# Kernel tuning notes

Measured on AMD Instinct MI355X. Metric: run time of the kernel, lower is better.

## Reference

```python
import jax, jax.numpy as jnp
import numpy as np

T, B, D = 4096, 64, 64
SCALE = D ** (-0.5)


def setup_inputs() -> dict:
    key = jax.random.key(0)
    ks = jax.random.split(key, 8)
    init = 1.0 / np.sqrt(D)  # mimic nn.Linear default scale roughly
    return {
        "eeg": jax.random.normal(ks[0], (T, B, D), dtype=jnp.float32),
        "fnirs": jax.random.normal(ks[1], (T, B, D), dtype=jnp.float32),
        "Wq": jax.random.normal(ks[2], (D, D), dtype=jnp.float32) * init,
        "bq": jax.random.normal(ks[3], (D,), dtype=jnp.float32) * init,
        "Wk": jax.random.normal(ks[4], (D, D), dtype=jnp.float32) * init,
        "bk": jax.random.normal(ks[5], (D,), dtype=jnp.float32) * init,
        "Wv": jax.random.normal(ks[6], (D, D), dtype=jnp.float32) * init,
        "bv": jax.random.normal(ks[7], (D,), dtype=jnp.float32) * init,
    }


def reference(eeg, fnirs, Wq, bq, Wk, bk, Wv, bv):
    # Linear layers: x @ W.T + b (torch nn.Linear convention, W is [out, in])
    q = jnp.einsum("tbd,od->tbo", eeg, Wq) + bq      # [T, B, D]
    k = jnp.einsum("tbd,od->tbo", fnirs, Wk) + bk    # [T, B, D]
    v = jnp.einsum("tbd,od->tbo", fnirs, Wv) + bv    # [T, B, D]
    # Elementwise QK gating score, summed over feature dim -> [T, B, 1]
    score = jnp.sum(q * k, axis=-1, keepdims=True) * SCALE
    # Softmax over the sequence axis (dim=0)
    attn = jax.nn.softmax(score, axis=0)
    # Residual combine
    return eeg + attn * v
```

## Files before the change

kernel.cpp:

```cpp
#include <hip/hip_runtime.h>
#include <hip/hip_bf16.h>
#include <math.h>

#define T_DIM 4096
#define B_DIM 64
#define NROWS (T_DIM * B_DIM)
#define NTILES (NROWS / 16)

#define WS_MFRAG 0
#define WS_VFRAG 2048
#define WS_U     4096
#define WS_W     4160
#define WS_C     4224
#define WS_MX    4240
#define WS_INV   4304
#define WS_PM    4368
#define WS_PS    8464
#define WS_SCORE 16384

typedef __attribute__((ext_vector_type(4))) float f32x4;
typedef __attribute__((ext_vector_type(8))) short bf16x8;

static __device__ inline short f2bf(float x) {
  __hip_bfloat16 h = __float2bfloat16(x);
  return *reinterpret_cast<short*>(&h);
}

static __device__ inline bf16x8 cvt8(const float4 a, const float4 b) {
  bf16x8 r;
  r[0] = f2bf(a.x); r[1] = f2bf(a.y); r[2] = f2bf(a.z); r[3] = f2bf(a.w);
  r[4] = f2bf(b.x); r[5] = f2bf(b.y); r[6] = f2bf(b.z); r[7] = f2bf(b.w);
  return r;
}

static __device__ inline float dot4(const float4 a, const float4 b, float acc) {
  acc = fmaf(a.x, b.x, acc); acc = fmaf(a.y, b.y, acc);
  acc = fmaf(a.z, b.z, acc); acc = fmaf(a.w, b.w, acc);
  return acc;
}

static __device__ __host__ inline int frag_idx(int d, int k) {
  return ((d >> 4) * 2 + (k >> 5)) * 512 +
         ((((k >> 3) & 3) * 16 + (d & 15)) * 8) + (k & 7);
}

__global__ __launch_bounds__(64) void k1_precompute(
    const float* __restrict__ Wq, const float* __restrict__ bq,
    const float* __restrict__ Wk, const float* __restrict__ bk,
    const float* __restrict__ Wv, float* __restrict__ ws) {
  const int tid = threadIdx.x;
  const int blk = blockIdx.x;
  unsigned short* __restrict__ mfrag = (unsigned short*)(ws + WS_MFRAG);
  unsigned short* __restrict__ vfrag = (unsigned short*)(ws + WS_VFRAG);
  if (blk < 64) {
    const int d = blk;
    float acc = 0.f;
#pragma unroll
    for (int o = 0; o < 64; ++o)
      acc = fmaf(Wq[o * 64 + d], Wk[o * 64 + tid], acc);
    const int idx = frag_idx(d, tid);
    mfrag[idx] = (unsigned short)f2bf(acc);
    vfrag[idx] = (unsigned short)f2bf(Wv[d * 64 + tid]);
  } else {
    float uacc = 0.f, wacc = 0.f, cacc = 0.f;
#pragma unroll
    for (int o = 0; o < 64; ++o) {
      uacc = fmaf(bq[o], Wk[o * 64 + tid], uacc);
      wacc = fmaf(Wq[o * 64 + tid], bk[o], wacc);
      cacc = fmaf(bq[o], bk[o], cacc);
    }
    ws[WS_U + tid] = uacc;
    ws[WS_W + tid] = wacc;
    if (tid == 0) ws[WS_C] = cacc;
  }
}

__global__ __launch_bounds__(256, 2) void k2_score_mfma(
    const float* __restrict__ eeg, const float* __restrict__ fnirs,
    const unsigned short* __restrict__ mfrag, const float* __restrict__ wvec,
    const float* __restrict__ uvec, const float* __restrict__ cvec,
    float* __restrict__ score) {
  __shared__ float lds[4][1024];
  const int tid = threadIdx.x;
  const int lane = tid & 63;
  const int wv = tid >> 6;
  const int tile = blockIdx.x * 4 + wv;
  const int c = lane & 15;
  const int g = lane >> 4;
  const int rbase = tile * 16;
  float* L = lds[wv];

  const float* Fb = fnirs + (size_t)rbase * 64;
  const float* Eb = eeg + (size_t)rbase * 64;
  float4 Fj[4], Ej[4];
#pragma unroll
  for (int j = 0; j < 4; ++j)
    Fj[j] = *reinterpret_cast<const float4*>(Fb + j * 256 + lane * 4);
#pragma unroll
  for (int j = 0; j < 4; ++j)
    Ej[j] = *reinterpret_cast<const float4*>(Eb + j * 256 + lane * 4);
  bf16x8 bm[4][2];
#pragma unroll
  for (int dt = 0; dt < 4; ++dt)
#pragma unroll
    for (int kf = 0; kf < 2; ++kf)
      bm[dt][kf] = *reinterpret_cast<const bf16x8*>(
          mfrag + (((dt * 2 + kf) << 9) + lane * 8));
  float4 wf[4];
#pragma unroll
  for (int dt = 0; dt < 4; ++dt)
    wf[dt] = *reinterpret_cast<const float4*>(wvec + dt * 16 + g * 4);
  const float4 u4 = *reinterpret_cast<const float4*>(uvec + c * 4);
  const float cb = cvec[0];
  __builtin_amdgcn_sched_barrier(0);

  float uf[4];
#pragma unroll
  for (int j = 0; j < 4; ++j) uf[j] = dot4(Fj[j], u4, 0.f);

#pragma unroll
  for (int j = 0; j < 4; ++j) {
    const int r = j * 4 + g;
    const int addr = r * 64 + ((((c >> 1) ^ (r & 7)) << 3) + ((c & 1) << 2));
    *reinterpret_cast<float4*>(&L[addr]) = Fj[j];
  }
  const int fr0 = c * 64 + (((g) ^ (c & 7)) << 3);
  const int fr1 = c * 64 + (((4 + g) ^ (c & 7)) << 3);
  const float4 p00 = *reinterpret_cast<const float4*>(&L[fr0]);
  const float4 p01 = *reinterpret_cast<const float4*>(&L[fr0 + 4]);
  const float4 p10 = *reinterpret_cast<const float4*>(&L[fr1]);
  const float4 p11 = *reinterpret_cast<const float4*>(&L[fr1 + 4]);
  const bf16x8 a0 = cvt8(p00, p01);
  const bf16x8 a1 = cvt8(p10, p11);

  const f32x4 zero = {0.f, 0.f, 0.f, 0.f};
  f32x4 acc[4];
#pragma unroll
  for (int dt = 0; dt < 4; ++dt) {
    acc[dt] = __builtin_amdgcn_mfma_f32_16x16x32_bf16(bm[dt][0], a0, zero, 0, 0, 0);
    acc[dt] = __builtin_amdgcn_mfma_f32_16x16x32_bf16(bm[dt][1], a1, acc[dt], 0, 0, 0);
  }

#pragma unroll
  for (int dt = 0; dt < 4; ++dt) {
    float4 hp;
    hp.x = acc[dt][0] + wf[dt].x; hp.y = acc[dt][1] + wf[dt].y;
    hp.z = acc[dt][2] + wf[dt].z; hp.w = acc[dt][3] + wf[dt].w;
    const int ch = dt * 2 + (g >> 1);
    const int addr = c * 64 + (((ch ^ (c & 7)) << 3) + ((g & 1) << 2));
    *reinterpret_cast<float4*>(&L[addr]) = hp;
  }
#pragma unroll
  for (int j = 0; j < 4; ++j) {
    const int r = j * 4 + g;
    const int addr = r * 64 + ((((c >> 1) ^ (r & 7)) << 3) + ((c & 1) << 2));
    const float4 hp = *reinterpret_cast<const float4*>(&L[addr]);
    float p = dot4(Ej[j], hp, uf[j]);
    p += __shfl_xor(p, 1, 64);
    p += __shfl_xor(p, 2, 64);
    p += __shfl_xor(p, 4, 64);
    p += __shfl_xor(p, 8, 64);
    if (c == 0) score[rbase + j * 4 + g] = (p + cb) * 0.125f;
  }
}

__global__ __launch_bounds__(256) void k3a_partial(
    const float* __restrict__ sc, float* __restrict__ pm,
    float* __restrict__ ps) {
  __shared__ float sm[4][64], ss[4][64];
  const int tid = threadIdx.x;
  const int b = tid & 63;
  const int tq = tid >> 6;
  const int t0 = blockIdx.x * 64;
  float m = -1e30f, s = 0.f;
#pragma unroll
  for (int k = 0; k < 16; ++k) {
    const float v = sc[(size_t)(t0 + k * 4 + tq) * 64 + b];
    const float mn = fmaxf(m, v);
    s = s * __expf(m - mn) + __expf(v - mn);
    m = mn;
  }
  sm[tq][b] = m; ss[tq][b] = s;
  __syncthreads();
  if (tid < 64) {
    float M = sm[0][b], S = ss[0][b];
#pragma unroll
    for (int w = 1; w < 4; ++w) {
      const float m2 = sm[w][b], s2 = ss[w][b];
      const float Mn = fmaxf(M, m2);
      S = S * __expf(M - Mn) + s2 * __expf(m2 - Mn);
      M = Mn;
    }
    pm[blockIdx.x * 64 + b] = M;
    ps[blockIdx.x * 64 + b] = S;
  }
}

__global__ __launch_bounds__(64) void k3b_combine(
    const float* __restrict__ pm, const float* __restrict__ ps,
    float* __restrict__ mx, float* __restrict__ inv) {
  const int b = threadIdx.x;
  float M = pm[b], S = ps[b];
#pragma unroll
  for (int ck = 1; ck < 64; ++ck) {
    const float m2 = pm[ck * 64 + b], s2 = ps[ck * 64 + b];
    const float Mn = fmaxf(M, m2);
    S = S * __expf(M - Mn) + s2 * __expf(m2 - Mn);
    M = Mn;
  }
  mx[b] = M;
  inv[b] = 1.0f / S;
}

__global__ __launch_bounds__(256, 2) void k4_output_mfma(
    const float* __restrict__ eeg, const float* __restrict__ fnirs,
    const unsigned short* __restrict__ vfrag, const float* __restrict__ bv,
    const float* __restrict__ score, const float* __restrict__ mx,
    const float* __restrict__ inv, float* __restrict__ out) {
  __shared__ float lds[4][1024];
  const int tid = threadIdx.x;
  const int lane = tid & 63;
  const int wv = tid >> 6;
  const int tile = blockIdx.x * 4 + wv;
  const int c = lane & 15;
  const int g = lane >> 4;
  const int rbase = tile * 16;
  float* L = lds[wv];

  const float* Fb = fnirs + (size_t)rbase * 64;
  const float* Eb = eeg + (size_t)rbase * 64;
  float4 Fj[4], Ej[4];
#pragma unroll
  for (int j = 0; j < 4; ++j)
    Fj[j] = *reinterpret_cast<const float4*>(Fb + j * 256 + lane * 4);
#pragma unroll
  for (int j = 0; j < 4; ++j)
    Ej[j] = *reinterpret_cast<const float4*>(Eb + j * 256 + lane * 4);
  bf16x8 bm[4][2];
#pragma unroll
  for (int dt = 0; dt < 4; ++dt)
#pragma unroll
    for (int kf = 0; kf < 2; ++kf)
      bm[dt][kf] = *reinterpret_cast<const bf16x8*>(
          vfrag + (((dt * 2 + kf) << 9) + lane * 8));
  float4 bvf[4];
#pragma unroll
  for (int dt = 0; dt < 4; ++dt)
    bvf[dt] = *reinterpret_cast<const float4*>(bv + dt * 16 + g * 4);
  const float scr = score[rbase + c];
  const int bidx = (rbase + c) & 63;
  const float mxv = mx[bidx];
  const float invv = inv[bidx];
  __builtin_amdgcn_sched_barrier(0);

#pragma unroll
  for (int j = 0; j < 4; ++j) {
    const int r = j * 4 + g;
    const int addr = r * 64 + ((((c >> 1) ^ (r & 7)) << 3) + ((c & 1) << 2));
    *reinterpret_cast<float4*>(&L[addr]) = Fj[j];
  }
  const int fr0 = c * 64 + (((g) ^ (c & 7)) << 3);
  const int fr1 = c * 64 + (((4 + g) ^ (c & 7)) << 3);
  const float4 p00 = *reinterpret_cast<const float4*>(&L[fr0]);
  const float4 p01 = *reinterpret_cast<const float4*>(&L[fr0 + 4]);
  const float4 p10 = *reinterpret_cast<const float4*>(&L[fr1]);
  const float4 p11 = *reinterpret_cast<const float4*>(&L[fr1 + 4]);
  const bf16x8 a0 = cvt8(p00, p01);
  const bf16x8 a1 = cvt8(p10, p11);

  const f32x4 zero = {0.f, 0.f, 0.f, 0.f};
  f32x4 acc[4];
#pragma unroll
  for (int dt = 0; dt < 4; ++dt) {
    acc[dt] = __builtin_amdgcn_mfma_f32_16x16x32_bf16(bm[dt][0], a0, zero, 0, 0, 0);
    acc[dt] = __builtin_amdgcn_mfma_f32_16x16x32_bf16(bm[dt][1], a1, acc[dt], 0, 0, 0);
  }

  const float aC = __expf(scr - mxv) * invv;
#pragma unroll
  for (int dt = 0; dt < 4; ++dt) {
    float4 v4;
    v4.x = aC * (acc[dt][0] + bvf[dt].x); v4.y = aC * (acc[dt][1] + bvf[dt].y);
    v4.z = aC * (acc[dt][2] + bvf[dt].z); v4.w = aC * (acc[dt][3] + bvf[dt].w);
    const int ch = dt * 2 + (g >> 1);
    const int addr = c * 64 + (((ch ^ (c & 7)) << 3) + ((g & 1) << 2));
    *reinterpret_cast<float4*>(&L[addr]) = v4;
  }
  float* Ob = out + (size_t)rbase * 64;
#pragma unroll
  for (int j = 0; j < 4; ++j) {
    const int r = j * 4 + g;
    const int addr = r * 64 + ((((c >> 1) ^ (r & 7)) << 3) + ((c & 1) << 2));
    const float4 v = *reinterpret_cast<const float4*>(&L[addr]);
    float4 o;
    o.x = Ej[j].x + v.x; o.y = Ej[j].y + v.y;
    o.z = Ej[j].z + v.z; o.w = Ej[j].w + v.w;
    *reinterpret_cast<float4*>(Ob + j * 256 + lane * 4) = o;
  }
}

extern "C" void kernel_launch(void* const* d_in, const int* in_sizes, int n_in,
                              void* d_out, int out_size, void* d_ws, size_t ws_size,
                              hipStream_t stream) {
  const float* eeg   = (const float*)d_in[0];
  const float* fnirs = (const float*)d_in[1];
  const float* Wq    = (const float*)d_in[2];
  const float* bq    = (const float*)d_in[3];
  const float* Wk    = (const float*)d_in[4];
  const float* bk    = (const float*)d_in[5];
  const float* Wv    = (const float*)d_in[6];
  const float* bv    = (const float*)d_in[7];
  float* out = (float*)d_out;
  float* ws  = (float*)d_ws;

  k1_precompute<<<65, 64, 0, stream>>>(Wq, bq, Wk, bk, Wv, ws);
  k2_score_mfma<<<NTILES / 4, 256, 0, stream>>>(
      eeg, fnirs, (const unsigned short*)(ws + WS_MFRAG), ws + WS_W,
      ws + WS_U, ws + WS_C, ws + WS_SCORE);
  k3a_partial<<<64, 256, 0, stream>>>(ws + WS_SCORE, ws + WS_PM, ws + WS_PS);
  k3b_combine<<<1, 64, 0, stream>>>(ws + WS_PM, ws + WS_PS,
                                    ws + WS_MX, ws + WS_INV);
  k4_output_mfma<<<NTILES / 4, 256, 0, stream>>>(
      eeg, fnirs, (const unsigned short*)(ws + WS_VFRAG), bv,
      ws + WS_SCORE, ws + WS_MX, ws + WS_INV, out);
}
```

Before: 66.65 us.

## Process four tiles per wave with double-buffered register prefetch in score and output kernels

Each wave in the score and output kernels now handles four consecutive 16-row tiles instead of one. The next tile's eeg/fnirs loads are issued before the current tile is computed, using two register buffers. This amortizes the per-wave setup (weight fragment and bias loads) and overlaps global memory latency with MFMA work. In exchange the grid is four times smaller and register pressure rises, which may reduce occupancy and the memory parallelism available across the GPU.

After: 69.50 us. 1.04x slower.

```diff
diff --git a/kernel.cpp b/kernel.cpp
--- a/kernel.cpp
+++ b/kernel.cpp
@@ -75,6 +75,62 @@
   }
 }
 
+
+#define K2_LOAD(Fj, Ej, t)                                                   \
+  {                                                                          \
+    const float* Fb_ = fnirs + (size_t)(t) * 1024;                           \
+    const float* Eb_ = eeg + (size_t)(t) * 1024;                             \
+    _Pragma("unroll") for (int j = 0; j < 4; ++j)                            \
+        Fj[j] = *reinterpret_cast<const float4*>(Fb_ + j * 256 + lane * 4);  \
+    _Pragma("unroll") for (int j = 0; j < 4; ++j)                            \
+        Ej[j] = *reinterpret_cast<const float4*>(Eb_ + j * 256 + lane * 4);  \
+  }
+
+#define K2_COMP(Fj, Ej, t)                                                   \
+  {                                                                          \
+    const int rbase_ = (t) * 16;                                             \
+    float uf_[4];                                                            \
+    _Pragma("unroll") for (int j = 0; j < 4; ++j)                            \
+        uf_[j] = dot4(Fj[j], u4, 0.f);                                       \
+    _Pragma("unroll") for (int j = 0; j < 4; ++j) {                          \
+      const int r_ = j * 4 + g;                                              \
+      const int a_ = r_ * 64 + ((((c >> 1) ^ (r_ & 7)) << 3) + ((c & 1) << 2)); \
+      *reinterpret_cast<float4*>(&L[a_]) = Fj[j];                            \
+    }                                                                        \
+    const int fr0_ = c * 64 + (((g) ^ (c & 7)) << 3);                        \
+    const int fr1_ = c * 64 + (((4 + g) ^ (c & 7)) << 3);                    \
+    const float4 p00_ = *reinterpret_cast<const float4*>(&L[fr0_]);          \
+    const float4 p01_ = *reinterpret_cast<const float4*>(&L[fr0_ + 4]);      \
+    const float4 p10_ = *reinterpret_cast<const float4*>(&L[fr1_]);          \
+    const float4 p11_ = *reinterpret_cast<const float4*>(&L[fr1_ + 4]);      \
+    const bf16x8 a0_ = cvt8(p00_, p01_);                                     \
+    const bf16x8 a1_ = cvt8(p10_, p11_);                                     \
+    f32x4 acc_[4];                                                           \
+    _Pragma("unroll") for (int dt = 0; dt < 4; ++dt) {                       \
+      acc_[dt] = __builtin_amdgcn_mfma_f32_16x16x32_bf16(bm[dt][0], a0_, zero, 0, 0, 0); \
+      acc_[dt] = __builtin_amdgcn_mfma_f32_16x16x32_bf16(bm[dt][1], a1_, acc_[dt], 0, 0, 0); \
+    }                                                                        \
+    _Pragma("unroll") for (int dt = 0; dt < 4; ++dt) {                       \
+      float4 hp_;                                                            \
+      hp_.x = acc_[dt][0] + wf[dt].x; hp_.y = acc_[dt][1] + wf[dt].y;        \
+      hp_.z = acc_[dt][2] + wf[dt].z; hp_.w = acc_[dt][3] + wf[dt].w;        \
+      const int ch_ = dt * 2 + (g >> 1);                                     \
+      const int a_ = c * 64 + (((ch_ ^ (c & 7)) << 3) + ((g & 1) << 2));     \
+      *reinterpret_cast<float4*>(&L[a_]) = hp_;                              \
+    }                                                                        \
+    _Pragma("unroll") for (int j = 0; j < 4; ++j) {                          \
+      const int r_ = j * 4 + g;                                              \
+      const int a_ = r_ * 64 + ((((c >> 1) ^ (r_ & 7)) << 3) + ((c & 1) << 2)); \
+      const float4 hp_ = *reinterpret_cast<const float4*>(&L[a_]);           \
+      float p_ = dot4(Ej[j], hp_, uf_[j]);                                   \
+      p_ += __shfl_xor(p_, 1, 64);                                           \
+      p_ += __shfl_xor(p_, 2, 64);                                           \
+      p_ += __shfl_xor(p_, 4, 64);                                           \
+      p_ += __shfl_xor(p_, 8, 64);                                           \
+      if (c == 0) score[rbase_ + j * 4 + g] = (p_ + cb) * 0.125f;            \
+    }                                                                        \
+  }
+
 __global__ __launch_bounds__(256, 2) void k2_score_mfma(
     const float* __restrict__ eeg, const float* __restrict__ fnirs,
     const unsigned short* __restrict__ mfrag, const float* __restrict__ wvec,
@@ -84,21 +140,12 @@
   const int tid = threadIdx.x;
   const int lane = tid & 63;
   const int wv = tid >> 6;
-  const int tile = blockIdx.x * 4 + wv;
+  const int wid = blockIdx.x * 4 + wv;
   const int c = lane & 15;
   const int g = lane >> 4;
-  const int rbase = tile * 16;
   float* L = lds[wv];
-
-  const float* Fb = fnirs + (size_t)rbase * 64;
-  const float* Eb = eeg + (size_t)rbase * 64;
-  float4 Fj[4], Ej[4];
-#pragma unroll
-  for (int j = 0; j < 4; ++j)
-    Fj[j] = *reinterpret_cast<const float4*>(Fb + j * 256 + lane * 4);
-#pragma unroll
-  for (int j = 0; j < 4; ++j)
-    Ej[j] = *reinterpret_cast<const float4*>(Eb + j * 256 + lane * 4);
+  const f32x4 zero = {0.f, 0.f, 0.f, 0.f};
+
   bf16x8 bm[4][2];
 #pragma unroll
   for (int dt = 0; dt < 4; ++dt)
@@ -112,56 +159,17 @@
     wf[dt] = *reinterpret_cast<const float4*>(wvec + dt * 16 + g * 4);
   const float4 u4 = *reinterpret_cast<const float4*>(uvec + c * 4);
   const float cb = cvec[0];
-  __builtin_amdgcn_sched_barrier(0);
-
-  float uf[4];
-#pragma unroll
-  for (int j = 0; j < 4; ++j) uf[j] = dot4(Fj[j], u4, 0.f);
-
-#pragma unroll
-  for (int j = 0; j < 4; ++j) {
-    const int r = j * 4 + g;
-    const int addr = r * 64 + ((((c >> 1) ^ (r & 7)) << 3) + ((c & 1) << 2));
-    *reinterpret_cast<float4*>(&L[addr]) = Fj[j];
-  }
-  const int fr0 = c * 64 + (((g) ^ (c & 7)) << 3);
-  const int fr1 = c * 64 + (((4 + g) ^ (c & 7)) << 3);
-  const float4 p00 = *reinterpret_cast<const float4*>(&L[fr0]);
-  const float4 p01 = *reinterpret_cast<const float4*>(&L[fr0 + 4]);
-  const float4 p10 = *reinterpret_cast<const float4*>(&L[fr1]);
-  const float4 p11 = *reinterpret_cast<const float4*>(&L[fr1 + 4]);
-  const bf16x8 a0 = cvt8(p00, p01);
-  const bf16x8 a1 = cvt8(p10, p11);
-
-  const f32x4 zero = {0.f, 0.f, 0.f, 0.f};
-  f32x4 acc[4];
-#pragma unroll
-  for (int dt = 0; dt < 4; ++dt) {
-    acc[dt] = __builtin_amdgcn_mfma_f32_16x16x32_bf16(bm[dt][0], a0, zero, 0, 0, 0);
-    acc[dt] = __builtin_amdgcn_mfma_f32_16x16x32_bf16(bm[dt][1], a1, acc[dt], 0, 0, 0);
-  }
-
-#pragma unroll
-  for (int dt = 0; dt < 4; ++dt) {
-    float4 hp;
-    hp.x = acc[dt][0] + wf[dt].x; hp.y = acc[dt][1] + wf[dt].y;
-    hp.z = acc[dt][2] + wf[dt].z; hp.w = acc[dt][3] + wf[dt].w;
-    const int ch = dt * 2 + (g >> 1);
-    const int addr = c * 64 + (((ch ^ (c & 7)) << 3) + ((g & 1) << 2));
-    *reinterpret_cast<float4*>(&L[addr]) = hp;
-  }
-#pragma unroll
-  for (int j = 0; j < 4; ++j) {
-    const int r = j * 4 + g;
-    const int addr = r * 64 + ((((c >> 1) ^ (r & 7)) << 3) + ((c & 1) << 2));
-    const float4 hp = *reinterpret_cast<const float4*>(&L[addr]);
-    float p = dot4(Ej[j], hp, uf[j]);
-    p += __shfl_xor(p, 1, 64);
-    p += __shfl_xor(p, 2, 64);
-    p += __shfl_xor(p, 4, 64);
-    p += __shfl_xor(p, 8, 64);
-    if (c == 0) score[rbase + j * 4 + g] = (p + cb) * 0.125f;
-  }
+
+  const int t0 = wid * 4;
+  float4 FA[4], EA[4], FB[4], EB[4];
+  K2_LOAD(FA, EA, t0);
+  K2_LOAD(FB, EB, t0 + 1);
+  K2_COMP(FA, EA, t0);
+  K2_LOAD(FA, EA, t0 + 2);
+  K2_COMP(FB, EB, t0 + 1);
+  K2_LOAD(FB, EB, t0 + 3);
+  K2_COMP(FA, EA, t0 + 2);
+  K2_COMP(FB, EB, t0 + 3);
 }
 
 __global__ __launch_bounds__(256) void k3a_partial(
@@ -212,6 +220,65 @@
   inv[b] = 1.0f / S;
 }
 
+
+#define K4_LOAD(Fj, Ej, scr, mxv, invv, t)                                   \
+  {                                                                          \
+    const float* Fb_ = fnirs + (size_t)(t) * 1024;                           \
+    const float* Eb_ = eeg + (size_t)(t) * 1024;                             \
+    _Pragma("unroll") for (int j = 0; j < 4; ++j)                            \
+        Fj[j] = *reinterpret_cast<const float4*>(Fb_ + j * 256 + lane * 4);  \
+    _Pragma("unroll") for (int j = 0; j < 4; ++j)                            \
+        Ej[j] = *reinterpret_cast<const float4*>(Eb_ + j * 256 + lane * 4);  \
+    scr = score[(t) * 16 + c];                                               \
+    const int b_ = ((t) * 16 + c) & 63;                                      \
+    mxv = mx[b_];                                                            \
+    invv = inv[b_];                                                          \
+  }
+
+#define K4_COMP(Fj, Ej, scr, mxv, invv, t)                                   \
+  {                                                                          \
+    const int rbase_ = (t) * 16;                                             \
+    _Pragma("unroll") for (int j = 0; j < 4; ++j) {                          \
+      const int r_ = j * 4 + g;                                              \
+      const int a_ = r_ * 64 + ((((c >> 1) ^ (r_ & 7)) << 3) + ((c & 1) << 2)); \
+      *reinterpret_cast<float4*>(&L[a_]) = Fj[j];                            \
+    }                                                                        \
+    const int fr0_ = c * 64 + (((g) ^ (c & 7)) << 3);                        \
+    const int fr1_ = c * 64 + (((4 + g) ^ (c & 7)) << 3);                    \
+    const float4 p00_ = *reinterpret_cast<const float4*>(&L[fr0_]);          \
+    const float4 p01_ = *reinterpret_cast<const float4*>(&L[fr0_ + 4]);      \
+    const float4 p10_ = *reinterpret_cast<const float4*>(&L[fr1_]);          \
+    const float4 p11_ = *reinterpret_cast<const float4*>(&L[fr1_ + 4]);      \
+    const bf16x8 a0_ = cvt8(p00_, p01_);                                     \
+    const bf16x8 a1_ = cvt8(p10_, p11_);                                     \
+    f32x4 acc_[4];                                                           \
+    _Pragma("unroll") for (int dt = 0; dt < 4; ++dt) {                       \
+      acc_[dt] = __builtin_amdgcn_mfma_f32_16x16x32_bf16(bm[dt][0], a0_, zero, 0, 0, 0); \
+      acc_[dt] = __builtin_amdgcn_mfma_f32_16x16x32_bf16(bm[dt][1], a1_, acc_[dt], 0, 0, 0); \
+    }                                                                        \
+    const float aC_ = __expf(scr - mxv) * invv;                              \
+    _Pragma("unroll") for (int dt = 0; dt < 4; ++dt) {                       \
+      float4 v4_;                                                            \
+      v4_.x = aC_ * (acc_[dt][0] + bvf[dt].x);                               \
+      v4_.y = aC_ * (acc_[dt][1] + bvf[dt].y);                               \
+      v4_.z = aC_ * (acc_[dt][2] + bvf[dt].z);                               \
+      v4_.w = aC_ * (acc_[dt][3] + bvf[dt].w);                               \
+      const int ch_ = dt * 2 + (g >> 1);                                     \
+      const int a_ = c * 64 + (((ch_ ^ (c & 7)) << 3) + ((g & 1) << 2));     \
+      *reinterpret_cast<float4*>(&L[a_]) = v4_;                              \
+    }                                                                        \
+    float* Ob_ = out + (size_t)rbase_ * 64;                                  \
+    _Pragma("unroll") for (int j = 0; j < 4; ++j) {                          \
+      const int r_ = j * 4 + g;                                              \
+      const int a_ = r_ * 64 + ((((c >> 1) ^ (r_ & 7)) << 3) + ((c & 1) << 2)); \
+      const float4 v_ = *reinterpret_cast<const float4*>(&L[a_]);            \
+      float4 o_;                                                             \
+      o_.x = Ej[j].x + v_.x; o_.y = Ej[j].y + v_.y;                          \
+      o_.z = Ej[j].z + v_.z; o_.w = Ej[j].w + v_.w;                          \
+      *reinterpret_cast<float4*>(Ob_ + j * 256 + lane * 4) = o_;             \
+    }                                                                        \
+  }
+
 __global__ __launch_bounds__(256, 2) void k4_output_mfma(
     const float* __restrict__ eeg, const float* __restrict__ fnirs,
     const unsigned short* __restrict__ vfrag, const float* __restrict__ bv,
@@ -221,21 +288,12 @@
   const int tid = threadIdx.x;
   const int lane = tid & 63;
   const int wv = tid >> 6;
-  const int tile = blockIdx.x * 4 + wv;
+  const int wid = blockIdx.x * 4 + wv;
   const int c = lane & 15;
   const int g = lane >> 4;
-  const int rbase = tile * 16;
   float* L = lds[wv];
-
-  const float* Fb = fnirs + (size_t)rbase * 64;
-  const float* Eb = eeg + (size_t)rbase * 64;
-  float4 Fj[4], Ej[4];
-#pragma unroll
-  for (int j = 0; j < 4; ++j)
-    Fj[j] = *reinterpret_cast<const float4*>(Fb + j * 256 + lane * 4);
-#pragma unroll
-  for (int j = 0; j < 4; ++j)
-    Ej[j] = *reinterpret_cast<const float4*>(Eb + j * 256 + lane * 4);
+  const f32x4 zero = {0.f, 0.f, 0.f, 0.f};
+
   bf16x8 bm[4][2];
 #pragma unroll
   for (int dt = 0; dt < 4; ++dt)
@@ -247,56 +305,18 @@
 #pragma unroll
   for (int dt = 0; dt < 4; ++dt)
     bvf[dt] = *reinterpret_cast<const float4*>(bv + dt * 16 + g * 4);
-  const float scr = score[rbase + c];
-  const int bidx = (rbase + c) & 63;
-  const float mxv = mx[bidx];
-  const float invv = inv[bidx];
-  __builtin_amdgcn_sched_barrier(0);
-
-#pragma unroll
-  for (int j = 0; j < 4; ++j) {
-    const int r = j * 4 + g;
-    const int addr = r * 64 + ((((c >> 1) ^ (r & 7)) << 3) + ((c & 1) << 2));
-    *reinterpret_cast<float4*>(&L[addr]) = Fj[j];
-  }
-  const int fr0 = c * 64 + (((g) ^ (c & 7)) << 3);
-  const int fr1 = c * 64 + (((4 + g) ^ (c & 7)) << 3);
-  const float4 p00 = *reinterpret_cast<const float4*>(&L[fr0]);
-  const float4 p01 = *reinterpret_cast<const float4*>(&L[fr0 + 4]);
-  const float4 p10 = *reinterpret_cast<const float4*>(&L[fr1]);
-  const float4 p11 = *reinterpret_cast<const float4*>(&L[fr1 + 4]);
-  const bf16x8 a0 = cvt8(p00, p01);
-  const bf16x8 a1 = cvt8(p10, p11);
-
-  const f32x4 zero = {0.f, 0.f, 0.f, 0.f};
-  f32x4 acc[4];
-#pragma unroll
-  for (int dt = 0; dt < 4; ++dt) {
-    acc[dt] = __builtin_amdgcn_mfma_f32_16x16x32_bf16(bm[dt][0], a0, zero, 0, 0, 0);
-    acc[dt] = __builtin_amdgcn_mfma_f32_16x16x32_bf16(bm[dt][1], a1, acc[dt], 0, 0, 0);
-  }
-
-  const float aC = __expf(scr - mxv) * invv;
-#pragma unroll
-  for (int dt = 0; dt < 4; ++dt) {
-    float4 v4;
-    v4.x = aC * (acc[dt][0] + bvf[dt].x); v4.y = aC * (acc[dt][1] + bvf[dt].y);
-    v4.z = aC * (acc[dt][2] + bvf[dt].z); v4.w = aC * (acc[dt][3] + bvf[dt].w);
-    const int ch = dt * 2 + (g >> 1);
-    const int addr = c * 64 + (((ch ^ (c & 7)) << 3) + ((g & 1) << 2));
-    *reinterpret_cast<float4*>(&L[addr]) = v4;
-  }
-  float* Ob = out + (size_t)rbase * 64;
-#pragma unroll
-  for (int j = 0; j < 4; ++j) {
-    const int r = j * 4 + g;
-    const int addr = r * 64 + ((((c >> 1) ^ (r & 7)) << 3) + ((c & 1) << 2));
-    const float4 v = *reinterpret_cast<const float4*>(&L[addr]);
-    float4 o;
-    o.x = Ej[j].x + v.x; o.y = Ej[j].y + v.y;
-    o.z = Ej[j].z + v.z; o.w = Ej[j].w + v.w;
-    *reinterpret_cast<float4*>(Ob + j * 256 + lane * 4) = o;
-  }
+
+  const int t0 = wid * 4;
+  float4 FA[4], EA[4], FB[4], EB[4];
+  float sA, mA, iA, sB, mB, iB;
+  K4_LOAD(FA, EA, sA, mA, iA, t0);
+  K4_LOAD(FB, EB, sB, mB, iB, t0 + 1);
+  K4_COMP(FA, EA, sA, mA, iA, t0);
+  K4_LOAD(FA, EA, sA, mA, iA, t0 + 2);
+  K4_COMP(FB, EB, sB, mB, iB, t0 + 1);
+  K4_LOAD(FB, EB, sB, mB, iB, t0 + 3);
+  K4_COMP(FA, EA, sA, mA, iA, t0 + 2);
+  K4_COMP(FB, EB, sB, mB, iB, t0 + 3);
 }
 
 extern "C" void kernel_launch(void* const* d_in, const int* in_sizes, int n_in,
@@ -314,13 +334,13 @@
   float* ws  = (float*)d_ws;
 
   k1_precompute<<<65, 64, 0, stream>>>(Wq, bq, Wk, bk, Wv, ws);
-  k2_score_mfma<<<NTILES / 4, 256, 0, stream>>>(
+  k2_score_mfma<<<NTILES / 16, 256, 0, stream>>>(
       eeg, fnirs, (const unsigned short*)(ws + WS_MFRAG), ws + WS_W,
       ws + WS_U, ws + WS_C, ws + WS_SCORE);
   k3a_partial<<<64, 256, 0, stream>>>(ws + WS_SCORE, ws + WS_PM, ws + WS_PS);
   k3b_combine<<<1, 64, 0, stream>>>(ws + WS_PM, ws + WS_PS,
                                     ws + WS_MX, ws + WS_INV);
-  k4_output_mfma<<<NTILES / 4, 256, 0, stream>>>(
+  k4_output_mfma<<<NTILES / 16, 256, 0, stream>>>(
       eeg, fnirs, (const unsigned short*)(ws + WS_VFRAG), bv,
       ws + WS_SCORE, ws + WS_MX, ws + WS_INV, out);
 }
```

## Double-buffer input tiles via direct global-to-LDS loads, four tiles per wave

Applied to the files above, without the earlier changes.

The score and output kernels now make each wave handle four 16-row tiles. They stage fnirs/eeg tiles into a double-buffered LDS region with global_load_lds and use manual vmcnt waits, so the next tile loads while the current one computes. Weight fragments and small vectors are copied once per block into LDS. The LDS round-trip transposes are replaced by a reduction across lanes. This is meant to hide memory latency and cut the per-tile fixed cost. In exchange it adds fragile hand-counted waitcnt values, more LDS per block (about 72KB), and fewer blocks.

Measured after the change: 70.90 us. +6.4%, slower.

```diff
diff --git a/kernel.cpp b/kernel.cpp
--- a/kernel.cpp
+++ b/kernel.cpp
@@ -42,6 +42,12 @@
 static __device__ __host__ inline int frag_idx(int d, int k) {
   return ((d >> 4) * 2 + (k >> 5)) * 512 +
          ((((k >> 3) & 3) * 16 + (d & 15)) * 8) + (k & 7);
+}
+
+static __device__ inline void gll16(const float* src, float* ldsbase) {
+  __builtin_amdgcn_global_load_lds(
+      (const __attribute__((address_space(1))) unsigned int*)src,
+      (__attribute__((address_space(3))) unsigned int*)ldsbase, 16, 0, 0);
 }
 
 __global__ __launch_bounds__(64) void k1_precompute(
@@ -75,93 +81,105 @@
   }
 }
 
+
+#define K2_STAGE(b_, t_)                                                      \
+  {                                                                           \
+    const size_t rb_ = (size_t)(t_) * 16;                                     \
+    float* Lb_ = &stg[wv][b_][0];                                             \
+    _Pragma("unroll") for (int q = 0; q < 4; ++q)                             \
+        gll16(fnirs + (rb_ + (lane & 15)) * 64 + (q * 4 + (lane >> 4)) * 4,   \
+              Lb_ + q * 256);                                                 \
+    _Pragma("unroll") for (int q = 0; q < 4; ++q)                             \
+        gll16(eeg + (rb_ + (lane & 15)) * 64 + (q * 4 + (lane >> 4)) * 4,     \
+              Lb_ + 1024 + q * 256);                                          \
+  }
+
+#define K2_COMP(b_, t_)                                                       \
+  {                                                                           \
+    const float* LF_ = &stg[wv][b_][0];                                       \
+    const float* LE_ = &stg[wv][b_][1024];                                    \
+    const float4 f0a_ = *reinterpret_cast<const float4*>(LF_ + (2 * g) * 64 + c * 4); \
+    const float4 f0b_ = *reinterpret_cast<const float4*>(LF_ + (2 * g + 1) * 64 + c * 4); \
+    const float4 f1a_ = *reinterpret_cast<const float4*>(LF_ + (8 + 2 * g) * 64 + c * 4); \
+    const float4 f1b_ = *reinterpret_cast<const float4*>(LF_ + (9 + 2 * g) * 64 + c * 4); \
+    float s_ = dot4(f0a_, u0a, dot4(f0b_, u0b, dot4(f1a_, u1a, dot4(f1b_, u1b, 0.f)))); \
+    const bf16x8 a0_ = cvt8(f0a_, f0b_);                                      \
+    const bf16x8 a1_ = cvt8(f1a_, f1b_);                                      \
+    f32x4 acc_[4];                                                            \
+    _Pragma("unroll") for (int dt = 0; dt < 4; ++dt) {                        \
+      acc_[dt] = __builtin_amdgcn_mfma_f32_16x16x32_bf16(bm[dt][0], a0_, zero, 0, 0, 0); \
+      acc_[dt] = __builtin_amdgcn_mfma_f32_16x16x32_bf16(bm[dt][1], a1_, acc_[dt], 0, 0, 0); \
+    }                                                                         \
+    _Pragma("unroll") for (int dt = 0; dt < 4; ++dt) {                        \
+      const float4 Ed_ = *reinterpret_cast<const float4*>(LE_ + (dt * 4 + g) * 64 + c * 4); \
+      float4 h_;                                                              \
+      h_.x = acc_[dt][0] + wfr[dt].x; h_.y = acc_[dt][1] + wfr[dt].y;         \
+      h_.z = acc_[dt][2] + wfr[dt].z; h_.w = acc_[dt][3] + wfr[dt].w;         \
+      s_ = dot4(Ed_, h_, s_);                                                 \
+    }                                                                         \
+    s_ += __shfl_xor(s_, 16, 64);                                             \
+    s_ += __shfl_xor(s_, 32, 64);                                             \
+    if (lane < 16) score[(t_) * 16 + lane] = (s_ + cb) * 0.125f;              \
+  }
+
 __global__ __launch_bounds__(256, 2) void k2_score_mfma(
     const float* __restrict__ eeg, const float* __restrict__ fnirs,
-    const unsigned short* __restrict__ mfrag, const float* __restrict__ wvec,
-    const float* __restrict__ uvec, const float* __restrict__ cvec,
-    float* __restrict__ score) {
-  __shared__ float lds[4][1024];
+    const float* __restrict__ wsf, float* __restrict__ score) {
+  __shared__ float stg[4][2][2048];
+  __shared__ unsigned short mw[4096];
+  __shared__ float wl[64];
+
   const int tid = threadIdx.x;
   const int lane = tid & 63;
   const int wv = tid >> 6;
-  const int tile = blockIdx.x * 4 + wv;
   const int c = lane & 15;
   const int g = lane >> 4;
-  const int rbase = tile * 16;
-  float* L = lds[wv];
-
-  const float* Fb = fnirs + (size_t)rbase * 64;
-  const float* Eb = eeg + (size_t)rbase * 64;
-  float4 Fj[4], Ej[4];
-#pragma unroll
-  for (int j = 0; j < 4; ++j)
-    Fj[j] = *reinterpret_cast<const float4*>(Fb + j * 256 + lane * 4);
-#pragma unroll
-  for (int j = 0; j < 4; ++j)
-    Ej[j] = *reinterpret_cast<const float4*>(Eb + j * 256 + lane * 4);
+
+  {
+    const float4* msrc = reinterpret_cast<const float4*>(wsf + WS_MFRAG);
+    float4* mdst = reinterpret_cast<float4*>(mw);
+    mdst[tid] = msrc[tid];
+    mdst[tid + 256] = msrc[tid + 256];
+    if (tid < 64) wl[tid] = wsf[WS_W + tid];
+  }
+  __syncthreads();
+
   bf16x8 bm[4][2];
 #pragma unroll
   for (int dt = 0; dt < 4; ++dt)
 #pragma unroll
     for (int kf = 0; kf < 2; ++kf)
       bm[dt][kf] = *reinterpret_cast<const bf16x8*>(
-          mfrag + (((dt * 2 + kf) << 9) + lane * 8));
-  float4 wf[4];
+          mw + (((dt * 2 + kf) << 9) + lane * 8));
+  float4 wfr[4];
 #pragma unroll
   for (int dt = 0; dt < 4; ++dt)
-    wf[dt] = *reinterpret_cast<const float4*>(wvec + dt * 16 + g * 4);
-  const float4 u4 = *reinterpret_cast<const float4*>(uvec + c * 4);
-  const float cb = cvec[0];
-  __builtin_amdgcn_sched_barrier(0);
-
-  float uf[4];
-#pragma unroll
-  for (int j = 0; j < 4; ++j) uf[j] = dot4(Fj[j], u4, 0.f);
-
-#pragma unroll
-  for (int j = 0; j < 4; ++j) {
-    const int r = j * 4 + g;
-    const int addr = r * 64 + ((((c >> 1) ^ (r & 7)) << 3) + ((c & 1) << 2));
-    *reinterpret_cast<float4*>(&L[addr]) = Fj[j];
-  }
-  const int fr0 = c * 64 + (((g) ^ (c & 7)) << 3);
-  const int fr1 = c * 64 + (((4 + g) ^ (c & 7)) << 3);
-  const float4 p00 = *reinterpret_cast<const float4*>(&L[fr0]);
-  const float4 p01 = *reinterpret_cast<const float4*>(&L[fr0 + 4]);
-  const float4 p10 = *reinterpret_cast<const float4*>(&L[fr1]);
-  const float4 p11 = *reinterpret_cast<const float4*>(&L[fr1 + 4]);
-  const bf16x8 a0 = cvt8(p00, p01);
-  const bf16x8 a1 = cvt8(p10, p11);
-
+    wfr[dt] = *reinterpret_cast<const float4*>(&wl[dt * 16 + g * 4]);
+  const float4 u0a = *reinterpret_cast<const float4*>(wsf + WS_U + g * 8);
+  const float4 u0b = *reinterpret_cast<const float4*>(wsf + WS_U + g * 8 + 4);
+  const float4 u1a = *reinterpret_cast<const float4*>(wsf + WS_U + 32 + g * 8);
+  const float4 u1b = *reinterpret_cast<const float4*>(wsf + WS_U + 36 + g * 8);
+  const float cb = wsf[WS_C];
   const f32x4 zero = {0.f, 0.f, 0.f, 0.f};
-  f32x4 acc[4];
-#pragma unroll
-  for (int dt = 0; dt < 4; ++dt) {
-    acc[dt] = __builtin_amdgcn_mfma_f32_16x16x32_bf16(bm[dt][0], a0, zero, 0, 0, 0);
-    acc[dt] = __builtin_amdgcn_mfma_f32_16x16x32_bf16(bm[dt][1], a1, acc[dt], 0, 0, 0);
-  }
-
-#pragma unroll
-  for (int dt = 0; dt < 4; ++dt) {
-    float4 hp;
-    hp.x = acc[dt][0] + wf[dt].x; hp.y = acc[dt][1] + wf[dt].y;
-    hp.z = acc[dt][2] + wf[dt].z; hp.w = acc[dt][3] + wf[dt].w;
-    const int ch = dt * 2 + (g >> 1);
-    const int addr = c * 64 + (((ch ^ (c & 7)) << 3) + ((g & 1) << 2));
-    *reinterpret_cast<float4*>(&L[addr]) = hp;
-  }
-#pragma unroll
-  for (int j = 0; j < 4; ++j) {
-    const int r = j * 4 + g;
-    const int addr = r * 64 + ((((c >> 1) ^ (r & 7)) << 3) + ((c & 1) << 2));
-    const float4 hp = *reinterpret_cast<const float4*>(&L[addr]);
-    float p = dot4(Ej[j], hp, uf[j]);
-    p += __shfl_xor(p, 1, 64);
-    p += __shfl_xor(p, 2, 64);
-    p += __shfl_xor(p, 4, 64);
-    p += __shfl_xor(p, 8, 64);
-    if (c == 0) score[rbase + j * 4 + g] = (p + cb) * 0.125f;
-  }
+
+  const int t0 = (blockIdx.x * 4 + wv) * 4;
+
+  K2_STAGE(0, t0);
+  K2_STAGE(1, t0 + 1);
+  asm volatile("s_waitcnt vmcnt(8)" ::: "memory");
+  __builtin_amdgcn_sched_barrier(0);
+  K2_COMP(0, t0);
+  K2_STAGE(0, t0 + 2);
+  asm volatile("s_waitcnt vmcnt(8)" ::: "memory");
+  __builtin_amdgcn_sched_barrier(0);
+  K2_COMP(1, t0 + 1);
+  K2_STAGE(1, t0 + 3);
+  asm volatile("s_waitcnt vmcnt(8)" ::: "memory");
+  __builtin_amdgcn_sched_barrier(0);
+  K2_COMP(0, t0 + 2);
+  asm volatile("s_waitcnt vmcnt(0)" ::: "memory");
+  __builtin_amdgcn_sched_barrier(0);
+  K2_COMP(1, t0 + 3);
 }
 
 __global__ __launch_bounds__(256) void k3a_partial(
@@ -212,91 +230,108 @@
   inv[b] = 1.0f / S;
 }
 
+
+#define K4_STAGE(b_, t_, scv_)                                                \
+  {                                                                           \
+    const size_t rb_ = (size_t)(t_) * 16;                                     \
+    float* Lb_ = &stg[wv][b_][0];                                             \
+    _Pragma("unroll") for (int q = 0; q < 4; ++q)                             \
+        gll16(fnirs + (rb_ + (lane & 15)) * 64 + (q * 4 + (lane >> 4)) * 4,   \
+              Lb_ + q * 256);                                                 \
+    _Pragma("unroll") for (int q = 0; q < 4; ++q)                             \
+        gll16(eeg + (rb_ + (lane & 15)) * 64 + (q * 4 + (lane >> 4)) * 4,     \
+              Lb_ + 1024 + q * 256);                                          \
+    scv_ = score[(t_) * 16 + c];                                              \
+  }
+
+#define K4_COMP(b_, t_, scv_)                                                 \
+  {                                                                           \
+    const float* LF_ = &stg[wv][b_][0];                                       \
+    const float* LE_ = &stg[wv][b_][1024];                                    \
+    const float4 f0a_ = *reinterpret_cast<const float4*>(LF_ + (2 * g) * 64 + c * 4); \
+    const float4 f0b_ = *reinterpret_cast<const float4*>(LF_ + (2 * g + 1) * 64 + c * 4); \
+    const float4 f1a_ = *reinterpret_cast<const float4*>(LF_ + (8 + 2 * g) * 64 + c * 4); \
+    const float4 f1b_ = *reinterpret_cast<const float4*>(LF_ + (9 + 2 * g) * 64 + c * 4); \
+    const bf16x8 a0_ = cvt8(f0a_, f0b_);                                      \
+    const bf16x8 a1_ = cvt8(f1a_, f1b_);                                      \
+    f32x4 acc_[4];                                                            \
+    _Pragma("unroll") for (int dt = 0; dt < 4; ++dt) {                        \
+      acc_[dt] = __builtin_amdgcn_mfma_f32_16x16x32_bf16(bm[dt][0], a0_, zero, 0, 0, 0); \
+      acc_[dt] = __builtin_amdgcn_mfma_f32_16x16x32_bf16(bm[dt][1], a1_, acc_[dt], 0, 0, 0); \
+    }                                                                         \
+    const int bl_ = (((t_) * 16) & 63) + c;                                   \
+    const float aC_ = __expf((scv_) - mxl[bl_]) * invl[bl_];                  \
+    float* ob_ = out + ((size_t)(t_) * 16 + c) * 64;                          \
+    _Pragma("unroll") for (int dt = 0; dt < 4; ++dt) {                        \
+      const float4 Ed_ = *reinterpret_cast<const float4*>(LE_ + (dt * 4 + g) * 64 + c * 4); \
+      float4 o_;                                                              \
+      o_.x = fmaf(aC_, acc_[dt][0] + bvf[dt].x, Ed_.x);                       \
+      o_.y = fmaf(aC_, acc_[dt][1] + bvf[dt].y, Ed_.y);                       \
+      o_.z = fmaf(aC_, acc_[dt][2] + bvf[dt].z, Ed_.z);                       \
+      o_.w = fmaf(aC_, acc_[dt][3] + bvf[dt].w, Ed_.w);                       \
+      *reinterpret_cast<float4*>(ob_ + dt * 16 + g * 4) = o_;                 \
+    }                                                                         \
+  }
+
 __global__ __launch_bounds__(256, 2) void k4_output_mfma(
     const float* __restrict__ eeg, const float* __restrict__ fnirs,
-    const unsigned short* __restrict__ vfrag, const float* __restrict__ bv,
-    const float* __restrict__ score, const float* __restrict__ mx,
-    const float* __restrict__ inv, float* __restrict__ out) {
-  __shared__ float lds[4][1024];
+    const float* __restrict__ wsf, const float* __restrict__ bv,
+    const float* __restrict__ score, float* __restrict__ out) {
+  __shared__ float stg[4][2][2048];
+  __shared__ unsigned short vw[4096];
+  __shared__ float bvl[64], mxl[64], invl[64];
+
   const int tid = threadIdx.x;
   const int lane = tid & 63;
   const int wv = tid >> 6;
-  const int tile = blockIdx.x * 4 + wv;
   const int c = lane & 15;
   const int g = lane >> 4;
-  const int rbase = tile * 16;
-  float* L = lds[wv];
-
-  const float* Fb = fnirs + (size_t)rbase * 64;
-  const float* Eb = eeg + (size_t)rbase * 64;
-  float4 Fj[4], Ej[4];
-#pragma unroll
-  for (int j = 0; j < 4; ++j)
-    Fj[j] = *reinterpret_cast<const float4*>(Fb + j * 256 + lane * 4);
-#pragma unroll
-  for (int j = 0; j < 4; ++j)
-    Ej[j] = *reinterpret_cast<const float4*>(Eb + j * 256 + lane * 4);
+
+  {
+    const float4* vsrc = reinterpret_cast<const float4*>(wsf + WS_VFRAG);
+    float4* vdst = reinterpret_cast<float4*>(vw);
+    vdst[tid] = vsrc[tid];
+    vdst[tid + 256] = vsrc[tid + 256];
+    if (tid < 64) {
+      bvl[tid] = bv[tid];
+      mxl[tid] = wsf[WS_MX + tid];
+      invl[tid] = wsf[WS_INV + tid];
+    }
+  }
+  __syncthreads();
+
   bf16x8 bm[4][2];
 #pragma unroll
   for (int dt = 0; dt < 4; ++dt)
 #pragma unroll
     for (int kf = 0; kf < 2; ++kf)
       bm[dt][kf] = *reinterpret_cast<const bf16x8*>(
-          vfrag + (((dt * 2 + kf) << 9) + lane * 8));
+          vw + (((dt * 2 + kf) << 9) + lane * 8));
   float4 bvf[4];
 #pragma unroll
   for (int dt = 0; dt < 4; ++dt)
-    bvf[dt] = *reinterpret_cast<const float4*>(bv + dt * 16 + g * 4);
-  const float scr = score[rbase + c];
-  const int bidx = (rbase + c) & 63;
-  const float mxv = mx[bidx];
-  const float invv = inv[bidx];
-  __builtin_amdgcn_sched_barrier(0);
-
-#pragma unroll
-  for (int j = 0; j < 4; ++j) {
-    const int r = j * 4 + g;
-    const int addr = r * 64 + ((((c >> 1) ^ (r & 7)) << 3) + ((c & 1) << 2));
-    *reinterpret_cast<float4*>(&L[addr]) = Fj[j];
-  }
-  const int fr0 = c * 64 + (((g) ^ (c & 7)) << 3);
-  const int fr1 = c * 64 + (((4 + g) ^ (c & 7)) << 3);
-  const float4 p00 = *reinterpret_cast<const float4*>(&L[fr0]);
-  const float4 p01 = *reinterpret_cast<const float4*>(&L[fr0 + 4]);
-  const float4 p10 = *reinterpret_cast<const float4*>(&L[fr1]);
-  const float4 p11 = *reinterpret_cast<const float4*>(&L[fr1 + 4]);
-  const bf16x8 a0 = cvt8(p00, p01);
-  const bf16x8 a1 = cvt8(p10, p11);
-
+    bvf[dt] = *reinterpret_cast<const float4*>(&bvl[dt * 16 + g * 4]);
   const f32x4 zero = {0.f, 0.f, 0.f, 0.f};
-  f32x4 acc[4];
-#pragma unroll
-  for (int dt = 0; dt < 4; ++dt) {
-    acc[dt] = __builtin_amdgcn_mfma_f32_16x16x32_bf16(bm[dt][0], a0, zero, 0, 0, 0);
-    acc[dt] = __builtin_amdgcn_mfma_f32_16x16x32_bf16(bm[dt][1], a1, acc[dt], 0, 0, 0);
-  }
-
-  const float aC = __expf(scr - mxv) * invv;
-#pragma unroll
-  for (int dt = 0; dt < 4; ++dt) {
-    float4 v4;
-    v4.x = aC * (acc[dt][0] + bvf[dt].x); v4.y = aC * (acc[dt][1] + bvf[dt].y);
-    v4.z = aC * (acc[dt][2] + bvf[dt].z); v4.w = aC * (acc[dt][3] + bvf[dt].w);
-    const int ch = dt * 2 + (g >> 1);
-    const int addr = c * 64 + (((ch ^ (c & 7)) << 3) + ((g & 1) << 2));
-    *reinterpret_cast<float4*>(&L[addr]) = v4;
-  }
-  float* Ob = out + (size_t)rbase * 64;
-#pragma unroll
-  for (int j = 0; j < 4; ++j) {
-    const int r = j * 4 + g;
-    const int addr = r * 64 + ((((c >> 1) ^ (r & 7)) << 3) + ((c & 1) << 2));
-    const float4 v = *reinterpret_cast<const float4*>(&L[addr]);
-    float4 o;
-    o.x = Ej[j].x + v.x; o.y = Ej[j].y + v.y;
-    o.z = Ej[j].z + v.z; o.w = Ej[j].w + v.w;
-    *reinterpret_cast<float4*>(Ob + j * 256 + lane * 4) = o;
-  }
+
+  const int t0 = (blockIdx.x * 4 + wv) * 4;
+  float scA, scB;
+
+  K4_STAGE(0, t0, scA);
+  K4_STAGE(1, t0 + 1, scB);
+  asm volatile("s_waitcnt vmcnt(9)" ::: "memory");
+  __builtin_amdgcn_sched_barrier(0);
+  K4_COMP(0, t0, scA);
+  K4_STAGE(0, t0 + 2, scA);
+  asm volatile("s_waitcnt vmcnt(9)" ::: "memory");
+  __builtin_amdgcn_sched_barrier(0);
+  K4_COMP(1, t0 + 1, scB);
+  K4_STAGE(1, t0 + 3, scB);
+  asm volatile("s_waitcnt vmcnt(9)" ::: "memory");
+  __builtin_amdgcn_sched_barrier(0);
+  K4_COMP(0, t0 + 2, scA);
+  asm volatile("s_waitcnt vmcnt(0)" ::: "memory");
+  __builtin_amdgcn_sched_barrier(0);
+  K4_COMP(1, t0 + 3, scB);
 }
 
 extern "C" void kernel_launch(void* const* d_in, const int* in_sizes, int n_in,
@@ -314,13 +349,10 @@
   float* ws  = (float*)d_ws;
 
   k1_precompute<<<65, 64, 0, stream>>>(Wq, bq, Wk, bk, Wv, ws);
-  k2_score_mfma<<<NTILES / 4, 256, 0, stream>>>(
-      eeg, fnirs, (const unsigned short*)(ws + WS_MFRAG), ws + WS_W,
-      ws + WS_U, ws + WS_C, ws + WS_SCORE);
+  k2_score_mfma<<<NTILES / 16, 256, 0, stream>>>(eeg, fnirs, ws, ws + WS_SCORE);
   k3a_partial<<<64, 256, 0, stream>>>(ws + WS_SCORE, ws + WS_PM, ws + WS_PS);
   k3b_combine<<<1, 64, 0, stream>>>(ws + WS_PM, ws + WS_PS,
                                     ws + WS_MX, ws + WS_INV);
-  k4_output_mfma<<<NTILES / 4, 256, 0, stream>>>(
-      eeg, fnirs, (const unsigned short*)(ws + WS_VFRAG), bv,
-      ws + WS_SCORE, ws + WS_MX, ws + WS_INV, out);
-}
+  k4_output_mfma<<<NTILES / 16, 256, 0, stream>>>(eeg, fnirs, ws, bv,
+                                                  ws + WS_SCORE, out);
+}
```
